# Performance work log

Hardware: AMD Instinct MI355X
Metric: run time of the kernel (lower is better)

## Reference

```python
import jax, jax.numpy as jnp
import numpy as np

H = 16
D_MODEL = 1024
D_K = D_MODEL // H


def setup_inputs() -> dict:
    key = jax.random.key(0)
    ks = jax.random.split(key, 11)
    B, S = 2, 2048
    scale = 1.0 / np.sqrt(D_MODEL)
    inp = {
        "query": jax.random.normal(ks[0], (B, S, D_MODEL), dtype=jnp.float32),
        "key": jax.random.normal(ks[1], (B, S, D_MODEL), dtype=jnp.float32),
        "value": jax.random.normal(ks[2], (B, S, D_MODEL), dtype=jnp.float32),
        "Wq": jax.random.normal(ks[3], (D_MODEL, D_MODEL), dtype=jnp.float32) * scale,
        "bq": jnp.zeros((D_MODEL,), dtype=jnp.float32),
        "Wk": jax.random.normal(ks[4], (D_MODEL, D_MODEL), dtype=jnp.float32) * scale,
        "bk": jnp.zeros((D_MODEL,), dtype=jnp.float32),
        "Wv": jax.random.normal(ks[5], (D_MODEL, D_MODEL), dtype=jnp.float32) * scale,
        "bv": jnp.zeros((D_MODEL,), dtype=jnp.float32),
        "Wo": jax.random.normal(ks[6], (D_MODEL, D_MODEL), dtype=jnp.float32) * scale,
        "bo": jnp.zeros((D_MODEL,), dtype=jnp.float32),
    }
    return inp


def _mha(query, key, value, Wq, bq, Wk, bk, Wv, bv, Wo, bo):
    B, S, _ = query.shape
    # linear projections (torch nn.Linear: x @ W.T + b)
    q = query @ Wq.T + bq
    k = key @ Wk.T + bk
    v = value @ Wv.T + bv
    # split heads: [B, S, D] -> [B, H, S, d_k]
    q = q.reshape(B, S, H, D_K).transpose(0, 2, 1, 3)
    k = k.reshape(B, S, H, D_K).transpose(0, 2, 1, 3)
    v = v.reshape(B, S, H, D_K).transpose(0, 2, 1, 3)
    # scaled dot-product attention with manual stable softmax
    scores = jnp.einsum("bhqd,bhkd->bhqk", q, k) / jnp.sqrt(jnp.float32(D_K))
    stable = scores - jnp.max(scores, axis=-1, keepdims=True)
    e = jnp.exp(stable)
    attn = e / jnp.sum(e, axis=-1, keepdims=True)
    ctx = jnp.einsum("bhqk,bhkd->bhqd", attn, v)
    # merge heads and final projection
    ctx = ctx.transpose(0, 2, 1, 3).reshape(B, S, H * D_K)
    return ctx @ Wo.T + bo


def reference(query, key, value, Wq, bq, Wk, bk, Wv, bv, Wo, bo):
    return _mha(query, key, value, Wq, bq, Wk, bk, Wv, bv, Wo, bo)
```

## Files before the change

kernel.cpp:

```cpp
#include <hip/hip_runtime.h>


#define S_LEN 2048
#define BATCH 2
#define DM    1024
#define NH    16
#define DKH   64
#define BS    (BATCH * S_LEN)

typedef _Float16 f16x8 __attribute__((ext_vector_type(8)));
typedef _Float16 f16x4 __attribute__((ext_vector_type(4)));
typedef _Float16 f16x2 __attribute__((ext_vector_type(2)));
typedef __fp16   h16x2 __attribute__((ext_vector_type(2)));
typedef float    f32x4 __attribute__((ext_vector_type(4)));
typedef float    f32x16 __attribute__((ext_vector_type(16)));

__device__ __forceinline__ f16x2 pk_f16(float a, float b) {
  h16x2 r = __builtin_amdgcn_cvt_pkrtz(a, b);
  return __builtin_bit_cast(f16x2, r);
}

__device__ __forceinline__ void gld16(const void* g, void* l) {
  __builtin_amdgcn_global_load_lds(
      (const __attribute__((address_space(1))) void*)g,
      (__attribute__((address_space(3))) void*)l, 16, 0, 0);
}

__device__ __forceinline__ float fast_exp2(float x) {
#if __has_builtin(__builtin_amdgcn_exp2f)
  return __builtin_amdgcn_exp2f(x);
#else
  return exp2f(x);
#endif
}

__device__ __forceinline__ int swap23(int x) {
  return (x & ~12) | ((x & 4) << 1) | ((x & 8) >> 1);
}

__global__ __launch_bounds__(256) void cvt_all(
    const float* __restrict__ q, const float* __restrict__ k, const float* __restrict__ v,
    const float* __restrict__ wq, const float* __restrict__ wk,
    const float* __restrict__ wv, const float* __restrict__ wo,
    _Float16* __restrict__ xq, _Float16* __restrict__ xk, _Float16* __restrict__ xv,
    _Float16* __restrict__ w16)
{
  const int y = blockIdx.y;
  const float* src; _Float16* dst; int n;
  if (y == 0)      { src = q;  dst = xq; n = BS * DM; }
  else if (y == 1) { src = k;  dst = xk; n = BS * DM; }
  else if (y == 2) { src = v;  dst = xv; n = BS * DM; }
  else {
    src = (y == 3) ? wq : ((y == 4) ? wk : ((y == 5) ? wv : wo));
    dst = w16 + (size_t)(y - 3) * (DM * DM);
    n = DM * DM;
  }
  int i0 = (blockIdx.x * 256 + threadIdx.x) * 4;
  if (i0 < n) {
    float4 f = *(const float4*)(src + i0);
    f16x2 lo = pk_f16(f.x, f.y);
    f16x2 hi = pk_f16(f.z, f.w);
    f16x4 hh; hh[0] = lo[0]; hh[1] = lo[1]; hh[2] = hi[0]; hh[3] = hi[1];
    *(f16x4*)(dst + i0) = hh;
  }
}

template <typename OUT_T, bool VT>
__device__ __forceinline__ void gemm_core(
    const _Float16* __restrict__ A, const _Float16* __restrict__ W,
    const float* __restrict__ bias, OUT_T* __restrict__ out, float oscale)
{
  const int tid  = threadIdx.x;
  const int l    = tid & 63;
  const int wv   = tid >> 6;
  const int c    = l & 15, quad = l >> 4;
  const int m0   = blockIdx.y * 128, n0 = blockIdx.x * 128;
  const int wm   = wv & 1, wn = wv >> 1;
  __shared__ _Float16 sA[128 * 64];
  __shared__ _Float16 sB[128 * 64];

  const _Float16* gA[4]; const _Float16* gB[4];
#pragma unroll
  for (int p = 0; p < 4; ++p) {
    int s = tid + p * 256, r = s >> 3, g = (s & 7) ^ (r & 7);
    gA[p] = A + (size_t)(m0 + r) * DM + g * 8;
    gB[p] = W + (size_t)(n0 + r) * DM + g * 8;
  }
  const int cx = c & 7;

  f32x4 acc[4][4] = {};
  for (int k0 = 0; k0 < DM; k0 += 64) {
    __syncthreads();
#pragma unroll
    for (int p = 0; p < 4; ++p) {
      gld16(gA[p] + k0, sA + (tid + p * 256) * 8);
      gld16(gB[p] + k0, sB + (tid + p * 256) * 8);
    }
    __syncthreads();
#pragma unroll
    for (int ks = 0; ks < 2; ++ks) {
      f16x8 af[4], bf[4];
#pragma unroll
      for (int i = 0; i < 4; ++i)
        af[i] = *(const f16x8*)&sA[(wm * 64 + i * 16 + c) * 64 + ((ks * 4 + quad) ^ cx) * 8];
#pragma unroll
      for (int j = 0; j < 4; ++j)
        bf[j] = *(const f16x8*)&sB[(wn * 64 + j * 16 + c) * 64 + ((ks * 4 + quad) ^ cx) * 8];
#pragma unroll
      for (int i = 0; i < 4; ++i)
#pragma unroll
        for (int j = 0; j < 4; ++j)
          acc[i][j] = __builtin_amdgcn_mfma_f32_16x16x32_f16(af[i], bf[j], acc[i][j], 0, 0, 0);
    }
  }
  if constexpr (VT) {
#pragma unroll
    for (int j = 0; j < 4; ++j) {
      int col = n0 + wn * 64 + j * 16 + c;
      float bb = bias[col];
      int hh = col >> 6, dd = col & 63;
#pragma unroll
      for (int i = 0; i < 4; ++i) {
        int row = m0 + wm * 64 + i * 16 + quad * 4;
        int bb2 = row >> 11, ss = row & (S_LEN - 1);
        _Float16* dst = (_Float16*)out + ((size_t)(bb2 * NH + hh) * DKH + dd) * S_LEN + ss;
        f16x4 v4;
#pragma unroll
        for (int r = 0; r < 4; ++r) v4[r] = (_Float16)((acc[i][j][r] + bb) * oscale);
        *(f16x4*)dst = v4;
      }
    }
  } else {
#pragma unroll
    for (int j = 0; j < 4; ++j) {
      int col = n0 + wn * 64 + j * 16 + c;
      float bb = bias[col];
#pragma unroll
      for (int i = 0; i < 4; ++i) {
        int row = m0 + wm * 64 + i * 16 + quad * 4;
#pragma unroll
        for (int r = 0; r < 4; ++r) {
          float vv = (acc[i][j][r] + bb) * oscale;
          out[(size_t)(row + r) * DM + col] = (OUT_T)vv;
        }
      }
    }
  }
}

#define SC_Q (0.125f * 1.44269504088896340736f)

__global__ __launch_bounds__(256) void proj3(
    const _Float16* __restrict__ xq, const _Float16* __restrict__ xk,
    const _Float16* __restrict__ xv, const _Float16* __restrict__ w16,
    const float* __restrict__ bq, const float* __restrict__ bk, const float* __restrict__ bv,
    _Float16* __restrict__ Q, _Float16* __restrict__ K, _Float16* __restrict__ Vt)
{
  const int z = blockIdx.z;
  if (z == 2) {
    gemm_core<_Float16, true>(xv, w16 + (size_t)2 * DM * DM, bv, Vt, 1.0f);
  } else if (z == 0) {
    gemm_core<_Float16, false>(xq, w16, bq, Q, SC_Q);
  } else {
    gemm_core<_Float16, false>(xk, w16 + (size_t)DM * DM, bk, K, 1.0f);
  }
}

__global__ __launch_bounds__(256) void out_gemm(
    const _Float16* __restrict__ ctx, const _Float16* __restrict__ wo,
    const float* __restrict__ bo, float* __restrict__ out)
{
  gemm_core<float, false>(ctx, wo, bo, out, 1.0f);
}

__global__ __launch_bounds__(256, 2) void attn(
    const _Float16* __restrict__ Q, const _Float16* __restrict__ K,
    const _Float16* __restrict__ Vt, _Float16* __restrict__ ctx)
{
  const int tid = threadIdx.x;
  const int l   = tid & 63, wv = tid >> 6;
  const int lo5 = l & 31, hf = l >> 5;
  const int wq  = wv >> 1, wk = wv & 1;
  const int q0  = blockIdx.x * 128;
  const int bh  = blockIdx.y;
  const int b   = bh >> 4, hd = bh & 15;
  __shared__ _Float16 sK[2][64 * 64];
  __shared__ _Float16 sV[2][64 * 64];

  f16x8 qf0[4], qf1[4];
  {
    const _Float16* Qg0 = Q + ((size_t)(b * S_LEN + q0 + wq * 64 + lo5)) * DM + hd * DKH + 8 * hf;
    const _Float16* Qg1 = Qg0 + (size_t)32 * DM;
#pragma unroll
    for (int kc = 0; kc < 4; ++kc) { qf0[kc] = *(const f16x8*)(Qg0 + 16 * kc);
                                     qf1[kc] = *(const f16x8*)(Qg1 + 16 * kc); }
  }

  f32x16 o0[2] = {}, o1[2] = {};
  float l0 = 0.f, l1 = 0.f;
  const f16x2 ones = {(_Float16)1.0f, (_Float16)1.0f};

  const _Float16* Kg0 = K + ((size_t)b * S_LEN) * DM + hd * DKH;
  const _Float16* Vg0 = Vt + ((size_t)bh * DKH) * S_LEN;

  const int sa = tid,       ra = sa >> 3, ba = (sa & 7) ^ (ra & 7);
  const int sb = tid + 256, rb = sb >> 3, bb = (sb & 7) ^ (rb & 7);
  const _Float16* gKa = Kg0 + (size_t)swap23(ra) * DM + ba * 8;
  const _Float16* gKb = Kg0 + (size_t)swap23(rb) * DM + bb * 8;
  const _Float16* gVa = Vg0 + (size_t)ra * S_LEN + ba * 8;
  const _Float16* gVb = Vg0 + (size_t)rb * S_LEN + bb * 8;
  const int rx = lo5 & 7;

#define STAGE(t, bf) do {                                   \
    const size_t k0s = (size_t)(t) * 64;                    \
    gld16(gKa + k0s * DM, sK[bf] + sa * 8);                 \
    gld16(gKb + k0s * DM, sK[bf] + sb * 8);                 \
    gld16(gVa + k0s,      sV[bf] + sa * 8);                 \
    gld16(gVb + k0s,      sV[bf] + sb * 8);                 \
  } while (0)

  STAGE(0, 0);
  asm volatile("s_waitcnt vmcnt(0)" ::: "memory");
  __builtin_amdgcn_s_barrier();

  const int NT = S_LEN / 64;
  for (int kt = 0; kt < NT; ++kt) {
    const int cur = kt & 1;
    if (kt + 1 < NT) STAGE(kt + 1, cur ^ 1);

    const _Float16* sKc = sK[cur];
    const _Float16* sVc = sV[cur];

    f32x16 sA0 = {}, sA1 = {};
    __builtin_amdgcn_s_setprio(1);
#pragma unroll
    for (int kc = 0; kc < 4; ++kc) {
      f16x8 kf = *(const f16x8*)&sKc[(32 * wk + lo5) * 64 + ((2 * kc + hf) ^ rx) * 8];
      sA0 = __builtin_amdgcn_mfma_f32_32x32x16_f16(kf, qf0[kc], sA0, 0, 0, 0);
      sA1 = __builtin_amdgcn_mfma_f32_32x32x16_f16(kf, qf1[kc], sA1, 0, 0, 0);
    }
    __builtin_amdgcn_s_setprio(0);

    f16x8 p0[2], p1[2];
#pragma unroll
    for (int half = 0; half < 2; ++half)
#pragma unroll
      for (int j2 = 0; j2 < 4; ++j2) {
        float a0 = fast_exp2(sA0[8 * half + 2 * j2]);
        float a1 = fast_exp2(sA0[8 * half + 2 * j2 + 1]);
        f16x2 pka = pk_f16(a0, a1);
        p0[half][2 * j2]     = pka[0];
        p0[half][2 * j2 + 1] = pka[1];
        l0 = __builtin_amdgcn_fdot2(__builtin_bit_cast(h16x2, pka),
                                    __builtin_bit_cast(h16x2, ones), l0, false);
        float b0 = fast_exp2(sA1[8 * half + 2 * j2]);
        float b1 = fast_exp2(sA1[8 * half + 2 * j2 + 1]);
        f16x2 pkb = pk_f16(b0, b1);
        p1[half][2 * j2]     = pkb[0];
        p1[half][2 * j2 + 1] = pkb[1];
        l1 = __builtin_amdgcn_fdot2(__builtin_bit_cast(h16x2, pkb),
                                    __builtin_bit_cast(h16x2, ones), l1, false);
      }

    __builtin_amdgcn_s_setprio(1);
#pragma unroll
    for (int db = 0; db < 2; ++db)
#pragma unroll
      for (int half = 0; half < 2; ++half) {
        const int kc2 = 2 * wk + half;
        f16x8 vf = *(const f16x8*)&sVc[(32 * db + lo5) * 64 + ((2 * kc2 + hf) ^ rx) * 8];
        o0[db] = __builtin_amdgcn_mfma_f32_32x32x16_f16(p0[half], vf, o0[db], 0, 0, 0);
        o1[db] = __builtin_amdgcn_mfma_f32_32x32x16_f16(p1[half], vf, o1[db], 0, 0, 0);
      }
    __builtin_amdgcn_s_setprio(0);

    if (kt + 1 < NT) {
      asm volatile("s_waitcnt vmcnt(0)" ::: "memory");
      __builtin_amdgcn_s_barrier();
    }
  }
#undef STAGE

  __syncthreads();

  l0 += __shfl_xor(l0, 32);
  l1 += __shfl_xor(l1, 32);
  float* lbuf = (float*)&sV[0][0];
  float* obuf = (float*)&sK[0][0];
  if (hf == 0) {
    lbuf[((wq * 2 + 0) * 2 + wk) * 32 + lo5] = l0;
    lbuf[((wq * 2 + 1) * 2 + wk) * 32 + lo5] = l1;
  }
  __syncthreads();

  float inv0[16], inv1[16];
#pragma unroll
  for (int r = 0; r < 16; ++r) {
    int qq = 8 * (r >> 2) + 4 * hf + (r & 3);
    inv0[r] = 1.0f / (lbuf[((wq * 2 + 0) * 2 + 0) * 32 + qq] +
                      lbuf[((wq * 2 + 0) * 2 + 1) * 32 + qq]);
    inv1[r] = 1.0f / (lbuf[((wq * 2 + 1) * 2 + 0) * 32 + qq] +
                      lbuf[((wq * 2 + 1) * 2 + 1) * 32 + qq]);
  }

  _Float16* Og = ctx + ((size_t)(b * S_LEN + q0 + wq * 64)) * DM + hd * DKH;
#pragma unroll
  for (int db = 0; db < 2; ++db) {
    if (wk == 1) {
#pragma unroll
      for (int r = 0; r < 16; ++r) {
        int qq = 8 * (r >> 2) + 4 * hf + (r & 3);
        obuf[((wq * 2 + 0) * 32 + qq) * 32 + lo5] = o0[db][r];
        obuf[((wq * 2 + 1) * 32 + qq) * 32 + lo5] = o1[db][r];
      }
    }
    __syncthreads();
    if (wk == 0) {
#pragma unroll
      for (int r = 0; r < 16; ++r) {
        int qq = 8 * (r >> 2) + 4 * hf + (r & 3);
        float v0 = o0[db][r] + obuf[((wq * 2 + 0) * 32 + qq) * 32 + lo5];
        float v1 = o1[db][r] + obuf[((wq * 2 + 1) * 32 + qq) * 32 + lo5];
        Og[(size_t)qq * DM + 32 * db + lo5]        = (_Float16)(v0 * inv0[r]);
        Og[(size_t)(32 + qq) * DM + 32 * db + lo5] = (_Float16)(v1 * inv1[r]);
      }
    }
    __syncthreads();
  }
}

extern "C" void kernel_launch(void* const* d_in, const int* in_sizes, int n_in,
                              void* d_out, int out_size, void* d_ws, size_t ws_size,
                              hipStream_t stream)
{
  (void)in_sizes; (void)n_in; (void)out_size; (void)ws_size;
  const float* q  = (const float*)d_in[0];
  const float* k  = (const float*)d_in[1];
  const float* v  = (const float*)d_in[2];
  const float* wq = (const float*)d_in[3];
  const float* bq = (const float*)d_in[4];
  const float* wk = (const float*)d_in[5];
  const float* bk = (const float*)d_in[6];
  const float* wv = (const float*)d_in[7];
  const float* bv = (const float*)d_in[8];
  const float* wo = (const float*)d_in[9];
  const float* bo = (const float*)d_in[10];

  char* ws = (char*)d_ws;
  _Float16* XQ  = (_Float16*)(ws);
  _Float16* XK  = (_Float16*)(ws + (8u  << 20));
  _Float16* XV  = (_Float16*)(ws + (16u << 20));
  _Float16* W16 = (_Float16*)(ws + (24u << 20));
  _Float16* Qp  = (_Float16*)(ws + (32u << 20));
  _Float16* Kp  = (_Float16*)(ws + (40u << 20));
  _Float16* VT  = (_Float16*)(ws + (48u << 20));
  _Float16* CTX = XQ;
  float* out = (float*)d_out;

  cvt_all<<<dim3(4096, 7), 256, 0, stream>>>(q, k, v, wq, wk, wv, wo, XQ, XK, XV, W16);
  proj3<<<dim3(8, 32, 3), 256, 0, stream>>>(XQ, XK, XV, W16, bq, bk, bv, Qp, Kp, VT);
  attn<<<dim3(16, 32), 256, 0, stream>>>(Qp, Kp, VT, CTX);
  out_gemm<<<dim3(8, 32), 256, 0, stream>>>(CTX, W16 + (size_t)3 * DM * DM, bo, out);
}
```

Baseline: 233.4 us.

## Give each attention wave private K/V LDS buffers and drop block barriers

Each of the four waves now loads its own 32-key slice of K and 32-column slice of V into a private double-buffered LDS region, so the per-tile workgroup barrier is replaced by per-wave vmcnt waits. This removes block-wide synchronisation from the attention inner loop, but K/V data shared by waves with the same wk is now fetched twice and LDS use per block stays the same. The grid is also transposed so consecutive blocks share the same batch-head, which may improve L2 reuse of K/V.

```diff
diff --git a/kernel.cpp b/kernel.cpp
--- a/kernel.cpp
+++ b/kernel.cpp
@@ -181,11 +181,12 @@
   const int l   = tid & 63, wv = tid >> 6;
   const int lo5 = l & 31, hf = l >> 5;
   const int wq  = wv >> 1, wk = wv & 1;
-  const int q0  = blockIdx.x * 128;
-  const int bh  = blockIdx.y;
+  const int bh  = blockIdx.x;
+  const int q0  = blockIdx.y * 128;
   const int b   = bh >> 4, hd = bh & 15;
-  __shared__ _Float16 sK[2][64 * 64];
-  __shared__ _Float16 sV[2][64 * 64];
+
+  __shared__ _Float16 sKw[4][2][32 * 64];
+  __shared__ _Float16 sVw[4][2][64 * 32];
 
   f16x8 qf0[4], qf1[4];
   {
@@ -203,39 +204,49 @@
   const _Float16* Kg0 = K + ((size_t)b * S_LEN) * DM + hd * DKH;
   const _Float16* Vg0 = Vt + ((size_t)bh * DKH) * S_LEN;
 
-  const int sa = tid,       ra = sa >> 3, ba = (sa & 7) ^ (ra & 7);
-  const int sb = tid + 256, rb = sb >> 3, bb = (sb & 7) ^ (rb & 7);
-  const _Float16* gKa = Kg0 + (size_t)swap23(ra) * DM + ba * 8;
-  const _Float16* gKb = Kg0 + (size_t)swap23(rb) * DM + bb * 8;
-  const _Float16* gVa = Vg0 + (size_t)ra * S_LEN + ba * 8;
-  const _Float16* gVb = Vg0 + (size_t)rb * S_LEN + bb * 8;
-  const int rx = lo5 & 7;
-
-#define STAGE(t, bf) do {                                   \
-    const size_t k0s = (size_t)(t) * 64;                    \
-    gld16(gKa + k0s * DM, sK[bf] + sa * 8);                 \
-    gld16(gKb + k0s * DM, sK[bf] + sb * 8);                 \
-    gld16(gVa + k0s,      sV[bf] + sa * 8);                 \
-    gld16(gVb + k0s,      sV[bf] + sb * 8);                 \
+  const _Float16* gK[4]; const _Float16* gV[4];
+#pragma unroll
+  for (int p = 0; p < 4; ++p) {
+    int s  = p * 64 + l;
+    int rk = s >> 3, gk = (s & 7) ^ (rk & 7);
+    gK[p] = Kg0 + (size_t)(32 * wk + swap23(rk)) * DM + gk * 8;
+    int rv = s >> 2, lv = (s & 3) ^ (rv & 3);
+    gV[p] = Vg0 + (size_t)rv * S_LEN + 32 * wk + lv * 8;
+  }
+  const int rx7 = lo5 & 7;
+  const int rx3 = lo5 & 3;
+
+  _Float16* kA = &sKw[wv][0][0]; _Float16* kB = &sKw[wv][1][0];
+  _Float16* vA = &sVw[wv][0][0]; _Float16* vB = &sVw[wv][1][0];
+
+#define STAGE(t, dK, dV) do {                               \
+    const size_t o = (size_t)(t) * 64;                      \
+    gld16(gK[0] + o * DM, (dK) + (l +   0) * 8);            \
+    gld16(gK[1] + o * DM, (dK) + (l +  64) * 8);            \
+    gld16(gK[2] + o * DM, (dK) + (l + 128) * 8);            \
+    gld16(gK[3] + o * DM, (dK) + (l + 192) * 8);            \
+    gld16(gV[0] + o,      (dV) + (l +   0) * 8);            \
+    gld16(gV[1] + o,      (dV) + (l +  64) * 8);            \
+    gld16(gV[2] + o,      (dV) + (l + 128) * 8);            \
+    gld16(gV[3] + o,      (dV) + (l + 192) * 8);            \
   } while (0)
 
-  STAGE(0, 0);
-  asm volatile("s_waitcnt vmcnt(0)" ::: "memory");
-  __builtin_amdgcn_s_barrier();
+  STAGE(0, kA, vA);
 
   const int NT = S_LEN / 64;
   for (int kt = 0; kt < NT; ++kt) {
-    const int cur = kt & 1;
-    if (kt + 1 < NT) STAGE(kt + 1, cur ^ 1);
-
-    const _Float16* sKc = sK[cur];
-    const _Float16* sVc = sV[cur];
+    if (kt + 1 < NT) {
+      STAGE(kt + 1, kB, vB);
+      asm volatile("s_waitcnt vmcnt(8)" ::: "memory");
+    } else {
+      asm volatile("s_waitcnt vmcnt(0)" ::: "memory");
+    }
 
     f32x16 sA0 = {}, sA1 = {};
     __builtin_amdgcn_s_setprio(1);
 #pragma unroll
     for (int kc = 0; kc < 4; ++kc) {
-      f16x8 kf = *(const f16x8*)&sKc[(32 * wk + lo5) * 64 + ((2 * kc + hf) ^ rx) * 8];
+      f16x8 kf = *(const f16x8*)&kA[lo5 * 64 + ((2 * kc + hf) ^ rx7) * 8];
       sA0 = __builtin_amdgcn_mfma_f32_32x32x16_f16(kf, qf0[kc], sA0, 0, 0, 0);
       sA1 = __builtin_amdgcn_mfma_f32_32x32x16_f16(kf, qf1[kc], sA1, 0, 0, 0);
     }
@@ -267,17 +278,14 @@
     for (int db = 0; db < 2; ++db)
 #pragma unroll
       for (int half = 0; half < 2; ++half) {
-        const int kc2 = 2 * wk + half;
-        f16x8 vf = *(const f16x8*)&sVc[(32 * db + lo5) * 64 + ((2 * kc2 + hf) ^ rx) * 8];
+        f16x8 vf = *(const f16x8*)&vA[(32 * db + lo5) * 32 + ((2 * half + hf) ^ rx3) * 8];
         o0[db] = __builtin_amdgcn_mfma_f32_32x32x16_f16(p0[half], vf, o0[db], 0, 0, 0);
         o1[db] = __builtin_amdgcn_mfma_f32_32x32x16_f16(p1[half], vf, o1[db], 0, 0, 0);
       }
     __builtin_amdgcn_s_setprio(0);
 
-    if (kt + 1 < NT) {
-      asm volatile("s_waitcnt vmcnt(0)" ::: "memory");
-      __builtin_amdgcn_s_barrier();
-    }
+    _Float16* t0 = kA; kA = kB; kB = t0;
+    _Float16* t1 = vA; vA = vB; vB = t1;
   }
 #undef STAGE
 
@@ -285,8 +293,8 @@
 
   l0 += __shfl_xor(l0, 32);
   l1 += __shfl_xor(l1, 32);
-  float* lbuf = (float*)&sV[0][0];
-  float* obuf = (float*)&sK[0][0];
+  float* lbuf = (float*)&sVw[0][0][0];
+  float* obuf = (float*)&sKw[0][0][0];
   if (hf == 0) {
     lbuf[((wq * 2 + 0) * 2 + wk) * 32 + lo5] = l0;
     lbuf[((wq * 2 + 1) * 2 + wk) * 32 + lo5] = l1;
@@ -359,6 +367,6 @@
 
   cvt_all<<<dim3(4096, 7), 256, 0, stream>>>(q, k, v, wq, wk, wv, wo, XQ, XK, XV, W16);
   proj3<<<dim3(8, 32, 3), 256, 0, stream>>>(XQ, XK, XV, W16, bq, bk, bv, Qp, Kp, VT);
-  attn<<<dim3(16, 32), 256, 0, stream>>>(Qp, Kp, VT, CTX);
+  attn<<<dim3(32, 16), 256, 0, stream>>>(Qp, Kp, VT, CTX);
   out_gemm<<<dim3(8, 32), 256, 0, stream>>>(CTX, W16 + (size_t)3 * DM * DM, bo, out);
 }
```

After: 233.8 us. About the same (+0.2%).

## Swap grid axes for block ordering and vectorize GEMM epilogue stores via transposed MFMA

Applied to the files above, without the earlier changes.

Reorders the grid dimensions of the projection, attention and output kernels so consecutive blocks walk along M (or along batch-head) rather than N or query tiles. This changes which A/W or K/V tiles are shared in cache by blocks running at the same time. For the non-VT GEMM path, the MFMA operands are swapped so each lane holds four consecutive output columns. The epilogue then issues 16-byte vector stores and a vector bias load instead of scalar strided stores. The aim is fewer global store transactions and better L2 locality, at the risk of different cache behaviour from the new block ordering.

```diff
diff --git a/kernel.cpp b/kernel.cpp
--- a/kernel.cpp
+++ b/kernel.cpp
@@ -74,7 +74,7 @@
   const int l    = tid & 63;
   const int wv   = tid >> 6;
   const int c    = l & 15, quad = l >> 4;
-  const int m0   = blockIdx.y * 128, n0 = blockIdx.x * 128;
+  const int m0   = blockIdx.x * 128, n0 = blockIdx.y * 128;
   const int wm   = wv & 1, wn = wv >> 1;
   __shared__ _Float16 sA[128 * 64];
   __shared__ _Float16 sB[128 * 64];
@@ -109,8 +109,12 @@
 #pragma unroll
       for (int i = 0; i < 4; ++i)
 #pragma unroll
-        for (int j = 0; j < 4; ++j)
-          acc[i][j] = __builtin_amdgcn_mfma_f32_16x16x32_f16(af[i], bf[j], acc[i][j], 0, 0, 0);
+        for (int j = 0; j < 4; ++j) {
+          if constexpr (VT)
+            acc[i][j] = __builtin_amdgcn_mfma_f32_16x16x32_f16(af[i], bf[j], acc[i][j], 0, 0, 0);
+          else
+            acc[j][i] = __builtin_amdgcn_mfma_f32_16x16x32_f16(bf[j], af[i], acc[j][i], 0, 0, 0);
+        }
     }
   }
   if constexpr (VT) {
@@ -133,15 +137,21 @@
   } else {
 #pragma unroll
     for (int j = 0; j < 4; ++j) {
-      int col = n0 + wn * 64 + j * 16 + c;
-      float bb = bias[col];
+      const int nb = n0 + wn * 64 + j * 16 + quad * 4;
+      const f32x4 bb = *(const f32x4*)(bias + nb);
 #pragma unroll
       for (int i = 0; i < 4; ++i) {
-        int row = m0 + wm * 64 + i * 16 + quad * 4;
-#pragma unroll
-        for (int r = 0; r < 4; ++r) {
-          float vv = (acc[i][j][r] + bb) * oscale;
-          out[(size_t)(row + r) * DM + col] = (OUT_T)vv;
+        const int m = m0 + wm * 64 + i * 16 + c;
+        if constexpr (__is_same(OUT_T, float)) {
+          f32x4 v4;
+#pragma unroll
+          for (int r = 0; r < 4; ++r) v4[r] = (acc[j][i][r] + bb[r]) * oscale;
+          *(f32x4*)((float*)out + (size_t)m * DM + nb) = v4;
+        } else {
+          f16x4 v4;
+#pragma unroll
+          for (int r = 0; r < 4; ++r) v4[r] = (_Float16)((acc[j][i][r] + bb[r]) * oscale);
+          *(f16x4*)((_Float16*)out + (size_t)m * DM + nb) = v4;
         }
       }
     }
@@ -181,8 +191,8 @@
   const int l   = tid & 63, wv = tid >> 6;
   const int lo5 = l & 31, hf = l >> 5;
   const int wq  = wv >> 1, wk = wv & 1;
-  const int q0  = blockIdx.x * 128;
-  const int bh  = blockIdx.y;
+  const int bh  = blockIdx.x;
+  const int q0  = blockIdx.y * 128;
   const int b   = bh >> 4, hd = bh & 15;
   __shared__ _Float16 sK[2][64 * 64];
   __shared__ _Float16 sV[2][64 * 64];
@@ -358,7 +368,7 @@
   float* out = (float*)d_out;
 
   cvt_all<<<dim3(4096, 7), 256, 0, stream>>>(q, k, v, wq, wk, wv, wo, XQ, XK, XV, W16);
-  proj3<<<dim3(8, 32, 3), 256, 0, stream>>>(XQ, XK, XV, W16, bq, bk, bv, Qp, Kp, VT);
-  attn<<<dim3(16, 32), 256, 0, stream>>>(Qp, Kp, VT, CTX);
-  out_gemm<<<dim3(8, 32), 256, 0, stream>>>(CTX, W16 + (size_t)3 * DM * DM, bo, out);
-}
+  proj3<<<dim3(32, 8, 3), 256, 0, stream>>>(XQ, XK, XV, W16, bq, bk, bv, Qp, Kp, VT);
+  attn<<<dim3(32, 16), 256, 0, stream>>>(Qp, Kp, VT, CTX);
+  out_gemm<<<dim3(32, 8), 256, 0, stream>>>(CTX, W16 + (size_t)3 * DM * DM, bo, out);
+}
```

After: 226.2 us. 1.03x faster.
